# Performance work log

Hardware: AMD Instinct MI355X
Metric: run time of the kernel (lower is better)

The kernel has to match this reference:

```python
import jax, jax.numpy as jnp
import numpy as np

B, N, D_PTS, D_MODEL, K = 2, 8192, 3, 128, 16


def _gather(points, idx):
    # points: (B, N, C), idx: (B, M, K) -> (B, M, K, C)
    return jax.vmap(lambda p, i: p[i])(points, idx)


def setup_inputs() -> dict:
    key = jax.random.key(0)
    ks = jax.random.split(key, 20)

    def w(k, shape, fan_in):
        bound = 1.0 / np.sqrt(fan_in)
        return jax.random.uniform(k, shape, jnp.float32, -bound, bound)

    return {
        "xyz": jax.random.normal(ks[0], (B, D_PTS, N), jnp.float32),
        "features": jax.random.normal(ks[1], (B, D_PTS, N), jnp.float32),
        "fc1_w": w(ks[2], (D_MODEL, D_PTS), D_PTS),
        "fc1_b": w(ks[3], (D_MODEL,), D_PTS),
        "fc2_w": w(ks[4], (D_PTS, D_MODEL), D_MODEL),
        "fc2_b": w(ks[5], (D_PTS,), D_MODEL),
        "d1_w": w(ks[6], (D_MODEL, 3), 3),
        "d1_b": w(ks[7], (D_MODEL,), 3),
        "d2_w": w(ks[8], (D_MODEL, D_MODEL), D_MODEL),
        "d2_b": w(ks[9], (D_MODEL,), D_MODEL),
        "g1_w": w(ks[10], (D_MODEL, D_MODEL), D_MODEL),
        "g1_b": w(ks[11], (D_MODEL,), D_MODEL),
        "g2_w": w(ks[12], (D_MODEL, D_MODEL), D_MODEL),
        "g2_b": w(ks[13], (D_MODEL,), D_MODEL),
        "wq_w": w(ks[14], (D_MODEL, D_MODEL), D_MODEL),
        "wk_w": w(ks[15], (D_MODEL, D_MODEL), D_MODEL),
        "wv_w": w(ks[16], (D_MODEL, D_MODEL), D_MODEL),
    }


def reference(xyz, features, fc1_w, fc1_b, fc2_w, fc2_b,
              d1_w, d1_b, d2_w, d2_b, g1_w, g1_b, g2_w, g2_b,
              wq_w, wk_w, wv_w):
    xyz_p = jnp.swapaxes(xyz, 1, 2)        # (B, N, 3)
    feat = jnp.swapaxes(features, 1, 2)    # (B, N, d_points)

    # square_distance(xyz, xyz): ||a||^2 + ||b||^2 - 2 a.b
    sq = jnp.sum(xyz_p * xyz_p, axis=-1)   # (B, N)
    dists = sq[:, :, None] + sq[:, None, :] - 2.0 * jnp.einsum('bnc,bmc->bnm', xyz_p, xyz_p)
    _, knn_idx = jax.lax.top_k(-dists, K)  # (B, N, K) indices of k smallest dists

    knn_xyz = _gather(xyz_p, knn_idx)      # (B, N, K, 3)
    pre = feat

    x = feat @ fc1_w.T + fc1_b             # (B, N, d_model)
    q = x @ wq_w.T                         # (B, N, d_model)
    kg = _gather(x @ wk_w.T, knn_idx)      # (B, N, K, d_model)
    vg = _gather(x @ wv_w.T, knn_idx)      # (B, N, K, d_model)

    rel = xyz_p[:, :, None] - knn_xyz      # (B, N, K, 3)
    pos = jax.nn.relu(rel @ d1_w.T + d1_b) @ d2_w.T + d2_b          # fc_delta

    h = q[:, :, None] - kg + pos
    attn = jax.nn.relu(h @ g1_w.T + g1_b) @ g2_w.T + g2_b           # fc_gamma
    attn = jax.nn.softmax(attn / np.sqrt(D_MODEL), axis=-2)         # softmax over K

    res = jnp.einsum('bmnf,bmnf->bmf', attn, vg + pos)              # (B, N, d_model)
    res = res @ fc2_w.T + fc2_b + pre                               # (B, N, d_points)
    return jnp.swapaxes(res, 1, 2)                                  # (B, d_points, N)
```

## Files before the change

kernel.cpp:

```cpp
#include <hip/hip_runtime.h>
#include <cfloat>

#define NPTS 8192

typedef __attribute__((ext_vector_type(8))) short short8;
typedef __attribute__((ext_vector_type(4))) short short4v;
typedef __attribute__((ext_vector_type(4))) float f32x4;

__device__ inline unsigned short f2bf(float f) {
    unsigned u = __builtin_bit_cast(unsigned, f);
    u += 0x7fffu + ((u >> 16) & 1u);
    return (unsigned short)(u >> 16);
}
__device__ inline float bf2f(unsigned short h) {
    unsigned u = ((unsigned)h) << 16;
    return __builtin_bit_cast(float, u);
}

__global__ void prep_kernel(const float* __restrict__ d2_w,
                            const float* __restrict__ g1_w,
                            const float* __restrict__ g2_w,
                            unsigned short* __restrict__ wd2,
                            unsigned short* __restrict__ wg1,
                            unsigned short* __restrict__ wg2,
                            const float* __restrict__ xyz,
                            float4* __restrict__ candp,
                            const float* __restrict__ wq_w,
                            const float* __restrict__ wk_w,
                            const float* __restrict__ wv_w,
                            float* __restrict__ wqT,
                            float* __restrict__ wkT,
                            float* __restrict__ wvT)
{
    int i = blockIdx.x * 256 + threadIdx.x;
    if (i < 49152) {
        int sel = i >> 14, off = i & 16383;
        const float* s = (sel == 0) ? d2_w : (sel == 1) ? g1_w : g2_w;
        unsigned short* d = (sel == 0) ? wd2 : (sel == 1) ? wg1 : wg2;
        d[off] = f2bf(s[off]);
    } else if (i < 65536) {
        int j = i - 49152;
        int b = j >> 13, n = j & 8191;
        const float* xg = xyz + (long)b * 3 * NPTS;
        float x = xg[n], y = xg[NPTS + n], z = xg[2*NPTS + n];
        float4 c; c.x = x; c.y = y; c.z = z;
        c.w = fmaf(x, x, fmaf(y, y, z * z));
        candp[j] = c;
    } else if (i < 114688) {
        int idx = i - 65536;
        int sel = idx >> 14, off = idx & 16383;
        int k = off >> 7, c = off & 127;
        const float* s = (sel == 0) ? wq_w : (sel == 1) ? wk_w : wv_w;
        float* d = (sel == 0) ? wqT : (sel == 1) ? wkT : wvT;
        d[off] = s[c * 128 + k];
    }
}

#define KNB 120
#define KBBASE 952
#define KCAP 64

__global__ __launch_bounds__(512, 2)
void knn_proj_kernel(const float4* __restrict__ cand,
                     float* __restrict__ part_d, int* __restrict__ part_i,
                     const float* __restrict__ feat,
                     const float* __restrict__ fc1_w, const float* __restrict__ fc1_b,
                     const float* __restrict__ wqT, const float* __restrict__ wkT,
                     const float* __restrict__ wvT,
                     unsigned short* __restrict__ qb,
                     unsigned short* __restrict__ kbuf,
                     unsigned short* __restrict__ vbuf)
{
    __shared__ union {
        struct {
            unsigned hist[KNB * 64];
            float2   surv[64 * 65];
            unsigned scnt[64];
            int      bthr[64];
        } k;
        struct {
            float fl[32][3];
            float xl[32][128];
        } p;
    } sm;

    const int t = threadIdx.x;

    if (blockIdx.x < 512) {
        unsigned* hist = sm.k.hist;
        float2*   surv = sm.k.surv;
        unsigned* scnt = sm.k.scnt;
        int*      bthr = sm.k.bthr;

        const int ql = t & 63, wv = t >> 6;
        const int wv_u = __builtin_amdgcn_readfirstlane(wv);
        const int qsg = blockIdx.x >> 1;
        const int ck  = blockIdx.x & 1;
        const int b_u = qsg >> 7;
        const int q   = qsg * 64 + ql;
        const int n   = q & 8191;

        const float4* cp = cand + (b_u << 13) + ck * 4096 + wv_u * 512;
        const int ibase = ck * 4096 + wv_u * 512;
        float4 qc = cand[(b_u << 13) + n];
        const float qx2 = -2.f * qc.x, qy2 = -2.f * qc.y, qz2 = -2.f * qc.z;
        const float qw = qc.w;

        for (int i = t; i < KNB * 64; i += 512) hist[i] = 0u;
        if (t < 64) scnt[t] = 0u;
        __syncthreads();

        auto dtil = [&](float4 c) {
            return fmaf(qx2, c.x, fmaf(qy2, c.y, fmaf(qz2, c.z, c.w + qw)));
        };
        auto binOf = [&](float d) {
            float dc = fmaxf(d, 1e-30f);
            int b = (int)(__builtin_bit_cast(unsigned, dc) >> 20) - KBBASE;
            return b < 0 ? 0 : (b > (KNB - 1) ? (KNB - 1) : b);
        };

        {
            unsigned* hq = hist + ql;
            float4 A[8], Bv[8];
            #pragma unroll
            for (int u = 0; u < 8; ++u) A[u] = cp[u];
            for (int m = 0; m < 512; m += 16) {
                #pragma unroll
                for (int u = 0; u < 8; ++u) Bv[u] = cp[m + 8 + u];
                #pragma unroll
                for (int u = 0; u < 8; ++u) {
                    int bb = binOf(dtil(A[u]));
                    atomicAdd(hq + bb * 64, 1u);
                }
                if (m + 16 < 512) {
                    #pragma unroll
                    for (int u = 0; u < 8; ++u) A[u] = cp[m + 16 + u];
                }
                #pragma unroll
                for (int u = 0; u < 8; ++u) {
                    int bb = binOf(dtil(Bv[u]));
                    atomicAdd(hq + bb * 64, 1u);
                }
            }
        }
        __syncthreads();

        if (t < 64) {
            int cum = 0, bs = 0;
            #pragma unroll 8
            for (int b = 0; b < KNB; ++b) {
                cum += (int)hist[b * 64 + t];
                bs += (cum < 16) ? 1 : 0;
            }
            bthr[t] = (bs >= KNB - 1) ? 0x7FFFFFFF : ((bs + KBBASE + 1) << 20);
        }
        __syncthreads();

        {
            const int mythr = bthr[ql];
            float4 A[8], Bv[8];
            #pragma unroll
            for (int u = 0; u < 8; ++u) A[u] = cp[u];
            for (int m = 0; m < 512; m += 16) {
                #pragma unroll
                for (int u = 0; u < 8; ++u) Bv[u] = cp[m + 8 + u];
                #pragma unroll
                for (int u = 0; u < 8; ++u) {
                    float d = dtil(A[u]);
                    if (__builtin_bit_cast(int, d) < mythr) {
                        unsigned s = atomicAdd(&scnt[ql], 1u);
                        if (s < (unsigned)KCAP) {
                            float2 e; e.x = d;
                            e.y = __builtin_bit_cast(float, ibase + m + u);
                            surv[ql * 65 + s] = e;
                        }
                    }
                }
                if (m + 16 < 512) {
                    #pragma unroll
                    for (int u = 0; u < 8; ++u) A[u] = cp[m + 16 + u];
                }
                #pragma unroll
                for (int u = 0; u < 8; ++u) {
                    float d = dtil(Bv[u]);
                    if (__builtin_bit_cast(int, d) < mythr) {
                        unsigned s = atomicAdd(&scnt[ql], 1u);
                        if (s < (unsigned)KCAP) {
                            float2 e; e.x = d;
                            e.y = __builtin_bit_cast(float, ibase + m + 8 + u);
                            surv[ql * 65 + s] = e;
                        }
                    }
                }
            }
        }
        __syncthreads();

        {
            const int q2 = t >> 3;
            const int s0 = t & 7;
            const unsigned cnt = min(scnt[q2], (unsigned)KCAP);
            const float2* sp = surv + q2 * 65;
            const long pb = ((long)(qsg * 64 + q2)) * 32 + ck * 16;
            for (unsigned s = s0; s < cnt; s += 8) {
                float2 e = sp[s];
                float d = e.x;
                int idx = __builtin_bit_cast(int, e.y);
                int rank = 0;
                #pragma unroll 8
                for (unsigned j = 0; j < cnt; ++j) {
                    float2 f = sp[j];
                    float dj = f.x;
                    int ij = __builtin_bit_cast(int, f.y);
                    rank += ((dj < d) || (dj == d && ij < idx)) ? 1 : 0;
                }
                if (rank < 16) {
                    part_d[pb + rank] = d;
                    part_i[pb + rank] = idx;
                }
            }
        }
    } else {
        float (*fl)[3]   = sm.p.fl;
        float (*xl)[128] = sm.p.xl;

        const int tc = t & 127;
        const int pg = t >> 7;
        const long base = (long)(blockIdx.x - 512) * 32 + pg * 8;

        if (tc < 24) {
            int p = tc / 3, d = tc % 3;
            long pt = base + p;
            int b = (int)(pt >> 13), n = (int)(pt & 8191);
            fl[pg*8 + p][d] = feat[((long)b * 3 + d) * NPTS + n];
        }
        __syncthreads();

        float w0 = fc1_w[tc*3+0], w1 = fc1_w[tc*3+1], w2 = fc1_w[tc*3+2];
        float b0 = fc1_b[tc];
        #pragma unroll
        for (int p = 0; p < 8; ++p)
            xl[pg*8 + p][tc] = fmaf(w0, fl[pg*8+p][0],
                               fmaf(w1, fl[pg*8+p][1],
                               fmaf(w2, fl[pg*8+p][2], b0)));
        __syncthreads();

        float aq[8], ak[8], av[8];
        #pragma unroll
        for (int p = 0; p < 8; ++p) { aq[p] = 0.f; ak[p] = 0.f; av[p] = 0.f; }

        for (int i4 = 0; i4 < 32; ++i4) {
            const int k0 = i4 * 4;
            float qa = wqT[(k0+0)*128 + tc], qbw = wqT[(k0+1)*128 + tc];
            float qc2 = wqT[(k0+2)*128 + tc], qd = wqT[(k0+3)*128 + tc];
            float ka = wkT[(k0+0)*128 + tc], kbw = wkT[(k0+1)*128 + tc];
            float kc2 = wkT[(k0+2)*128 + tc], kd = wkT[(k0+3)*128 + tc];
            float va = wvT[(k0+0)*128 + tc], vbw = wvT[(k0+1)*128 + tc];
            float vc2 = wvT[(k0+2)*128 + tc], vd = wvT[(k0+3)*128 + tc];
            #pragma unroll
            for (int p = 0; p < 8; ++p) {
                float4 x = *(const float4*)&xl[pg*8 + p][k0];
                aq[p] = fmaf(qa,x.x, fmaf(qbw,x.y, fmaf(qc2,x.z, fmaf(qd,x.w, aq[p]))));
                ak[p] = fmaf(ka,x.x, fmaf(kbw,x.y, fmaf(kc2,x.z, fmaf(kd,x.w, ak[p]))));
                av[p] = fmaf(va,x.x, fmaf(vbw,x.y, fmaf(vc2,x.z, fmaf(vd,x.w, av[p]))));
            }
        }
        const int perm = (tc & 15) * 8 + (tc >> 4);
        #pragma unroll
        for (int p = 0; p < 8; ++p) {
            long pt = base + p;
            qb[pt*128 + perm]   = f2bf(aq[p]);
            kbuf[pt*128 + perm] = f2bf(ak[p]);
            vbuf[pt*128 + perm] = f2bf(av[p]);
        }
    }
}

__global__ __launch_bounds__(256, 4)
void knn_merge_kernel(const float* __restrict__ part_d,
                      const int* __restrict__ part_i, int* __restrict__ knn)
{
    __shared__ float sd[8][33];
    __shared__ int   si[8][33];
    const int t = threadIdx.x;
    const int qq = t >> 5, e = t & 31;
    const long q = (long)blockIdx.x * 8 + qq;
    float d = part_d[q * 32 + e];
    int idx = part_i[q * 32 + e];
    sd[qq][e] = d; si[qq][e] = idx;
    __syncthreads();
    int rank = 0;
    #pragma unroll
    for (int j = 0; j < 32; ++j) {
        float dj = sd[qq][j];
        rank += ((dj < d) || (dj == d && si[qq][j] < idx)) ? 1 : 0;
    }
    if (rank < 16) knn[q * 16 + rank] = idx;
}

__device__ inline int hswz(int r, int c) {
    return r * 128 + (c ^ ((r & 7) << 4));
}

__global__ __launch_bounds__(64, 2)
void attn_kernel(const float* __restrict__ xyz, const float* __restrict__ feat,
                 const float* __restrict__ d1_w, const float* __restrict__ d1_b,
                 const float* __restrict__ d2_b, const float* __restrict__ g1_b,
                 const float* __restrict__ g2_b,
                 const float* __restrict__ fc2_w, const float* __restrict__ fc2_b,
                 const unsigned short* __restrict__ qb,
                 const unsigned short* __restrict__ kb,
                 const unsigned short* __restrict__ vb,
                 const unsigned short* __restrict__ wd2,
                 const unsigned short* __restrict__ wg1,
                 const unsigned short* __restrict__ wg2,
                 const int* __restrict__ knn, float* __restrict__ out)
{
    __shared__ unsigned short hbuf[32 * 128];

    const int lane = threadIdx.x;
    const int quad = lane >> 4, l15 = lane & 15;
    const long pbase = (long)blockIdx.x * 2;
    const int b = (int)(pbase >> 13);
    const long bofs = (long)b * NPTS;

    int m = 0; float rx = 0.f, ry = 0.f, rz = 0.f;
    if (lane < 32) {
        m = knn[(pbase + (lane >> 4)) * 16 + (lane & 15)];
        int nn = (int)((pbase + (lane >> 4)) & 8191);
        const float* xg = xyz + (long)b * 3 * NPTS;
        rx = xg[nn]        - xg[m];
        ry = xg[NPTS+nn]   - xg[NPTS+m];
        rz = xg[2*NPTS+nn] - xg[2*NPTS+m];
    }

    int koff[8];
    #pragma unroll
    for (int mt = 0; mt < 2; ++mt)
        #pragma unroll
        for (int r = 0; r < 4; ++r) {
            int idxm = __shfl(m, mt*16 + quad*4 + r);
            koff[mt*4 + r] = (int)(bofs + idxm) * 128 + l15*8;
        }

    short8 qvv[2], kgv[2][4], vgv[2][4];
    #pragma unroll
    for (int mt = 0; mt < 2; ++mt) {
        qvv[mt] = *(const short8*)(qb + (size_t)(pbase + mt) * 128 + l15*8);
        #pragma unroll
        for (int r = 0; r < 4; ++r)
            kgv[mt][r] = *(const short8*)(kb + koff[mt*4 + r]);
    }

    {
        float w0[8], w1[8], w2[8], bb[8];
        #pragma unroll
        for (int k = 0; k < 8; ++k) {
            int c = l15*8 + k;
            w0[k] = d1_w[c*3]; w1[k] = d1_w[c*3+1]; w2[k] = d1_w[c*3+2];
            bb[k] = d1_b[c];
        }
        #pragma unroll
        for (int i = 0; i < 8; ++i) {
            int row = quad + 4*i;
            float sx = __shfl(rx, row), sy = __shfl(ry, row), sz = __shfl(rz, row);
            short8 hv;
            #pragma unroll
            for (int k = 0; k < 8; ++k) {
                float v = fmaf(w0[k], sx, fmaf(w1[k], sy, fmaf(w2[k], sz, bb[k])));
                hv[k] = (short)f2bf(fmaxf(v, 0.f));
            }
            *(short8*)&hbuf[hswz(row, l15*8)] = hv;
        }
    }

    short8 A[2][4];
    f32x4 acc[2];

    auto loadA = [&]() {
        #pragma unroll
        for (int mt = 0; mt < 2; ++mt)
            #pragma unroll
            for (int kk = 0; kk < 4; ++kk)
                A[mt][kk] = *(const short8*)&hbuf[hswz(mt*16 + l15, kk*32 + quad*8)];
    };

    unsigned posp[2][8][2];

    loadA();
    #pragma unroll
    for (int n0 = 0; n0 < 8; ++n0) {
        const unsigned short* wp = wd2 + (n0*16 + l15) * 128 + quad*8;
        short8 B0 = *(const short8*)(wp);
        short8 B1 = *(const short8*)(wp + 32);
        short8 B2 = *(const short8*)(wp + 64);
        short8 B3 = *(const short8*)(wp + 96);
        acc[0] = (f32x4){0.f,0.f,0.f,0.f};
        acc[1] = (f32x4){0.f,0.f,0.f,0.f};
        __builtin_amdgcn_s_setprio(1);
        #pragma unroll
        for (int mt = 0; mt < 2; ++mt) {
            acc[mt] = __builtin_amdgcn_mfma_f32_16x16x32_bf16(A[mt][0], B0, acc[mt], 0, 0, 0);
            acc[mt] = __builtin_amdgcn_mfma_f32_16x16x32_bf16(A[mt][1], B1, acc[mt], 0, 0, 0);
            acc[mt] = __builtin_amdgcn_mfma_f32_16x16x32_bf16(A[mt][2], B2, acc[mt], 0, 0, 0);
            acc[mt] = __builtin_amdgcn_mfma_f32_16x16x32_bf16(A[mt][3], B3, acc[mt], 0, 0, 0);
        }
        __builtin_amdgcn_s_setprio(0);
        int c = n0*16 + l15;
        float bb = d2_b[c];
        #pragma unroll
        for (int mt = 0; mt < 2; ++mt) {
            float qv = bf2f((unsigned short)qvv[mt][n0]);
            float p0 = acc[mt][0] + bb, p1 = acc[mt][1] + bb;
            float p2 = acc[mt][2] + bb, p3 = acc[mt][3] + bb;
            posp[mt][n0][0] = (unsigned)f2bf(p0) | ((unsigned)f2bf(p1) << 16);
            posp[mt][n0][1] = (unsigned)f2bf(p2) | ((unsigned)f2bf(p3) << 16);
            int rb = mt*16 + quad*4;
            hbuf[hswz(rb+0, c)] = f2bf(qv - bf2f((unsigned short)kgv[mt][0][n0]) + p0);
            hbuf[hswz(rb+1, c)] = f2bf(qv - bf2f((unsigned short)kgv[mt][1][n0]) + p1);
            hbuf[hswz(rb+2, c)] = f2bf(qv - bf2f((unsigned short)kgv[mt][2][n0]) + p2);
            hbuf[hswz(rb+3, c)] = f2bf(qv - bf2f((unsigned short)kgv[mt][3][n0]) + p3);
        }
    }

    loadA();
    #pragma unroll
    for (int n0 = 0; n0 < 8; ++n0) {
        const unsigned short* wp = wg1 + (n0*16 + l15) * 128 + quad*8;
        short8 B0 = *(const short8*)(wp);
        short8 B1 = *(const short8*)(wp + 32);
        short8 B2 = *(const short8*)(wp + 64);
        short8 B3 = *(const short8*)(wp + 96);
        acc[0] = (f32x4){0.f,0.f,0.f,0.f};
        acc[1] = (f32x4){0.f,0.f,0.f,0.f};
        __builtin_amdgcn_s_setprio(1);
        #pragma unroll
        for (int mt = 0; mt < 2; ++mt) {
            acc[mt] = __builtin_amdgcn_mfma_f32_16x16x32_bf16(A[mt][0], B0, acc[mt], 0, 0, 0);
            acc[mt] = __builtin_amdgcn_mfma_f32_16x16x32_bf16(A[mt][1], B1, acc[mt], 0, 0, 0);
            acc[mt] = __builtin_amdgcn_mfma_f32_16x16x32_bf16(A[mt][2], B2, acc[mt], 0, 0, 0);
            acc[mt] = __builtin_amdgcn_mfma_f32_16x16x32_bf16(A[mt][3], B3, acc[mt], 0, 0, 0);
        }
        __builtin_amdgcn_s_setprio(0);
        int c = n0*16 + l15;
        float bb = g1_b[c];
        #pragma unroll
        for (int mt = 0; mt < 2; ++mt) {
            int rb = mt*16 + quad*4;
            #pragma unroll
            for (int r = 0; r < 4; ++r)
                hbuf[hswz(rb+r, c)] = f2bf(fmaxf(acc[mt][r] + bb, 0.f));
        }
    }

    #pragma unroll
    for (int mt = 0; mt < 2; ++mt)
        #pragma unroll
        for (int r = 0; r < 4; ++r)
            vgv[mt][r] = *(const short8*)(vb + koff[mt*4 + r]);

    loadA();
    const float sc = 0.08838834764831845f;
    float pr[2][3];
    #pragma unroll
    for (int mt = 0; mt < 2; ++mt) { pr[mt][0] = 0.f; pr[mt][1] = 0.f; pr[mt][2] = 0.f; }
    #pragma unroll
    for (int n0 = 0; n0 < 8; ++n0) {
        const unsigned short* wp = wg2 + (n0*16 + l15) * 128 + quad*8;
        short8 B0 = *(const short8*)(wp);
        short8 B1 = *(const short8*)(wp + 32);
        short8 B2 = *(const short8*)(wp + 64);
        short8 B3 = *(const short8*)(wp + 96);
        acc[0] = (f32x4){0.f,0.f,0.f,0.f};
        acc[1] = (f32x4){0.f,0.f,0.f,0.f};
        __builtin_amdgcn_s_setprio(1);
        #pragma unroll
        for (int mt = 0; mt < 2; ++mt) {
            acc[mt] = __builtin_amdgcn_mfma_f32_16x16x32_bf16(A[mt][0], B0, acc[mt], 0, 0, 0);
            acc[mt] = __builtin_amdgcn_mfma_f32_16x16x32_bf16(A[mt][1], B1, acc[mt], 0, 0, 0);
            acc[mt] = __builtin_amdgcn_mfma_f32_16x16x32_bf16(A[mt][2], B2, acc[mt], 0, 0, 0);
            acc[mt] = __builtin_amdgcn_mfma_f32_16x16x32_bf16(A[mt][3], B3, acc[mt], 0, 0, 0);
        }
        __builtin_amdgcn_s_setprio(0);
        int c = n0*16 + l15;
        float bb = g2_b[c];
        float f0 = fc2_w[c];
        float f1 = fc2_w[128 + c];
        float f2 = fc2_w[256 + c];
        #pragma unroll
        for (int mt = 0; mt < 2; ++mt) {
            float e0 = (acc[mt][0] + bb) * sc;
            float e1 = (acc[mt][1] + bb) * sc;
            float e2 = (acc[mt][2] + bb) * sc;
            float e3 = (acc[mt][3] + bb) * sc;
            float mx = fmaxf(fmaxf(e0, e1), fmaxf(e2, e3));
            mx = fmaxf(mx, __shfl_xor(mx, 16));
            mx = fmaxf(mx, __shfl_xor(mx, 32));
            e0 = __expf(e0 - mx); e1 = __expf(e1 - mx);
            e2 = __expf(e2 - mx); e3 = __expf(e3 - mx);
            float ssum = e0 + e1 + e2 + e3;
            ssum += __shfl_xor(ssum, 16);
            ssum += __shfl_xor(ssum, 32);
            float p0 = bf2f((unsigned short)(posp[mt][n0][0] & 0xffff));
            float p1 = bf2f((unsigned short)(posp[mt][n0][0] >> 16));
            float p2 = bf2f((unsigned short)(posp[mt][n0][1] & 0xffff));
            float p3 = bf2f((unsigned short)(posp[mt][n0][1] >> 16));
            float p = e0 * (bf2f((unsigned short)vgv[mt][0][n0]) + p0)
                    + e1 * (bf2f((unsigned short)vgv[mt][1][n0]) + p1)
                    + e2 * (bf2f((unsigned short)vgv[mt][2][n0]) + p2)
                    + e3 * (bf2f((unsigned short)vgv[mt][3][n0]) + p3);
            p += __shfl_xor(p, 16);
            p += __shfl_xor(p, 32);
            float rres = p / ssum;
            pr[mt][0] = fmaf(f0, rres, pr[mt][0]);
            pr[mt][1] = fmaf(f1, rres, pr[mt][1]);
            pr[mt][2] = fmaf(f2, rres, pr[mt][2]);
        }
    }

    #pragma unroll
    for (int mt = 0; mt < 2; ++mt) {
        float pr0 = pr[mt][0], pr1 = pr[mt][1], pr2 = pr[mt][2];
        #pragma unroll
        for (int s2 = 1; s2 <= 8; s2 <<= 1) {
            pr0 += __shfl_xor(pr0, s2);
            pr1 += __shfl_xor(pr1, s2);
            pr2 += __shfl_xor(pr2, s2);
        }
        int nn = (int)((pbase + mt) & 8191);
        if (lane < 3) {
            float pv = (lane == 0) ? pr0 : (lane == 1) ? pr1 : pr2;
            long o = ((long)b*3 + lane) * NPTS + nn;
            out[o] = pv + fc2_b[lane] + feat[o];
        }
    }
}

extern "C" void kernel_launch(void* const* d_in, const int* in_sizes, int n_in,
                              void* d_out, int out_size, void* d_ws, size_t ws_size,
                              hipStream_t stream)
{
    const float* xyz   = (const float*)d_in[0];
    const float* feat  = (const float*)d_in[1];
    const float* fc1_w = (const float*)d_in[2];
    const float* fc1_b = (const float*)d_in[3];
    const float* fc2_w = (const float*)d_in[4];
    const float* fc2_b = (const float*)d_in[5];
    const float* d1_w  = (const float*)d_in[6];
    const float* d1_b  = (const float*)d_in[7];
    const float* d2_w  = (const float*)d_in[8];
    const float* d2_b  = (const float*)d_in[9];
    const float* g1_w  = (const float*)d_in[10];
    const float* g1_b  = (const float*)d_in[11];
    const float* g2_w  = (const float*)d_in[12];
    const float* g2_b  = (const float*)d_in[13];
    const float* wq_w  = (const float*)d_in[14];
    const float* wk_w  = (const float*)d_in[15];
    const float* wv_w  = (const float*)d_in[16];
    float* out = (float*)d_out;

    unsigned short* qb  = (unsigned short*)d_ws;
    unsigned short* kb  = qb + (size_t)16384*128;
    unsigned short* vb  = kb + (size_t)16384*128;
    unsigned short* wd2 = vb + (size_t)16384*128;
    unsigned short* wg1 = wd2 + 16384;
    unsigned short* wg2 = wg1 + 16384;
    int*   knn_ws = (int*)(wg2 + 16384);
    float4* cand  = (float4*)(knn_ws + (size_t)16384*16);
    float* part_d = (float*)(cand + 16384);
    int*   part_i = (int*)(part_d + (size_t)16384*64);
    float* wqT    = part_d + (size_t)16384*32;
    float* wkT    = wqT + 16384;
    float* wvT    = wkT + 16384;

    hipLaunchKernelGGL(prep_kernel, dim3(448), dim3(256), 0, stream,
                       d2_w, g1_w, g2_w, wd2, wg1, wg2, xyz, cand,
                       wq_w, wk_w, wv_w, wqT, wkT, wvT);
    hipLaunchKernelGGL(knn_proj_kernel, dim3(1024), dim3(512), 0, stream,
                       cand, part_d, part_i,
                       feat, fc1_w, fc1_b, wqT, wkT, wvT, qb, kb, vb);
    hipLaunchKernelGGL(knn_merge_kernel, dim3(2048), dim3(256), 0, stream,
                       part_d, part_i, knn_ws);
    hipLaunchKernelGGL(attn_kernel, dim3(8192), dim3(64), 0, stream,
                       xyz, feat, d1_w, d1_b, d2_b, g1_b, g2_b, fc2_w, fc2_b,
                       qb, kb, vb, wd2, wg1, wg2, knn_ws, out);
}
```

Measured before the change: 296.6 us.

## Split KNN partial pass into own kernel and fuse merge with QKV projection

The KNN partial-selection pass moves into its own kernel with launch bounds (512,6) and no shared-memory union with the projection path. The QKV projection blocks, now processing 16 points per 256-thread block, join the KNN merge kernel in a single launch. This lets the KNN kernel run at higher occupancy without carrying the projection's shared-memory footprint. The merge and the projection can overlap in one launch. It trades this against losing the previous overlap of projection with the histogram KNN pass.

```diff
diff --git a/kernel.cpp b/kernel.cpp
--- a/kernel.cpp
+++ b/kernel.cpp
@@ -60,179 +60,188 @@
 #define KBBASE 952
 #define KCAP 64
 
-__global__ __launch_bounds__(512, 2)
-void knn_proj_kernel(const float4* __restrict__ cand,
-                     float* __restrict__ part_d, int* __restrict__ part_i,
-                     const float* __restrict__ feat,
-                     const float* __restrict__ fc1_w, const float* __restrict__ fc1_b,
-                     const float* __restrict__ wqT, const float* __restrict__ wkT,
-                     const float* __restrict__ wvT,
-                     unsigned short* __restrict__ qb,
-                     unsigned short* __restrict__ kbuf,
-                     unsigned short* __restrict__ vbuf)
+__global__ __launch_bounds__(512, 6)
+void knn_part_kernel(const float4* __restrict__ cand,
+                     float* __restrict__ part_d, int* __restrict__ part_i)
+{
+    __shared__ unsigned hist[KNB * 64];
+    __shared__ float2   surv[64 * 65];
+    __shared__ unsigned scnt[64];
+    __shared__ int      bthr[64];
+
+    const int t  = threadIdx.x;
+    const int ql = t & 63, wv = t >> 6;
+    const int wv_u = __builtin_amdgcn_readfirstlane(wv);
+    const int qsg = blockIdx.x >> 1;
+    const int ck  = blockIdx.x & 1;
+    const int b_u = qsg >> 7;
+    const int q   = qsg * 64 + ql;
+    const int n   = q & 8191;
+
+    const float4* cp = cand + (b_u << 13) + ck * 4096 + wv_u * 512;
+    const int ibase = ck * 4096 + wv_u * 512;
+    float4 qc = cand[(b_u << 13) + n];
+    const float qx2 = -2.f * qc.x, qy2 = -2.f * qc.y, qz2 = -2.f * qc.z;
+    const float qw = qc.w;
+
+    for (int i = t; i < KNB * 64; i += 512) hist[i] = 0u;
+    if (t < 64) scnt[t] = 0u;
+    __syncthreads();
+
+    auto dtil = [&](float4 c) {
+        return fmaf(qx2, c.x, fmaf(qy2, c.y, fmaf(qz2, c.z, c.w + qw)));
+    };
+    auto binOf = [&](float d) {
+        float dc = fmaxf(d, 1e-30f);
+        int b = (int)(__builtin_bit_cast(unsigned, dc) >> 20) - KBBASE;
+        return b < 0 ? 0 : (b > (KNB - 1) ? (KNB - 1) : b);
+    };
+
+    {
+        unsigned* hq = hist + ql;
+        float4 A[8], Bv[8];
+        #pragma unroll
+        for (int u = 0; u < 8; ++u) A[u] = cp[u];
+        for (int m = 0; m < 512; m += 16) {
+            #pragma unroll
+            for (int u = 0; u < 8; ++u) Bv[u] = cp[m + 8 + u];
+            #pragma unroll
+            for (int u = 0; u < 8; ++u) {
+                int bb = binOf(dtil(A[u]));
+                atomicAdd(hq + bb * 64, 1u);
+            }
+            if (m + 16 < 512) {
+                #pragma unroll
+                for (int u = 0; u < 8; ++u) A[u] = cp[m + 16 + u];
+            }
+            #pragma unroll
+            for (int u = 0; u < 8; ++u) {
+                int bb = binOf(dtil(Bv[u]));
+                atomicAdd(hq + bb * 64, 1u);
+            }
+        }
+    }
+    __syncthreads();
+
+    if (t < 64) {
+        int cum = 0, bs = 0;
+        #pragma unroll 8
+        for (int b = 0; b < KNB; ++b) {
+            cum += (int)hist[b * 64 + t];
+            bs += (cum < 16) ? 1 : 0;
+        }
+        bthr[t] = (bs >= KNB - 1) ? 0x7FFFFFFF : ((bs + KBBASE + 1) << 20);
+    }
+    __syncthreads();
+
+    {
+        const int mythr = bthr[ql];
+        float4 A[8], Bv[8];
+        #pragma unroll
+        for (int u = 0; u < 8; ++u) A[u] = cp[u];
+        for (int m = 0; m < 512; m += 16) {
+            #pragma unroll
+            for (int u = 0; u < 8; ++u) Bv[u] = cp[m + 8 + u];
+            #pragma unroll
+            for (int u = 0; u < 8; ++u) {
+                float d = dtil(A[u]);
+                if (__builtin_bit_cast(int, d) < mythr) {
+                    unsigned s = atomicAdd(&scnt[ql], 1u);
+                    if (s < (unsigned)KCAP) {
+                        float2 e; e.x = d;
+                        e.y = __builtin_bit_cast(float, ibase + m + u);
+                        surv[ql * 65 + s] = e;
+                    }
+                }
+            }
+            if (m + 16 < 512) {
+                #pragma unroll
+                for (int u = 0; u < 8; ++u) A[u] = cp[m + 16 + u];
+            }
+            #pragma unroll
+            for (int u = 0; u < 8; ++u) {
+                float d = dtil(Bv[u]);
+                if (__builtin_bit_cast(int, d) < mythr) {
+                    unsigned s = atomicAdd(&scnt[ql], 1u);
+                    if (s < (unsigned)KCAP) {
+                        float2 e; e.x = d;
+                        e.y = __builtin_bit_cast(float, ibase + m + 8 + u);
+                        surv[ql * 65 + s] = e;
+                    }
+                }
+            }
+        }
+    }
+    __syncthreads();
+
+    {
+        const int q2 = t >> 3;
+        const int s0 = t & 7;
+        const unsigned cnt = min(scnt[q2], (unsigned)KCAP);
+        const float2* sp = surv + q2 * 65;
+        const long pb = ((long)(qsg * 64 + q2)) * 32 + ck * 16;
+        for (unsigned s = s0; s < cnt; s += 8) {
+            float2 e = sp[s];
+            float d = e.x;
+            int idx = __builtin_bit_cast(int, e.y);
+            int rank = 0;
+            #pragma unroll 8
+            for (unsigned j = 0; j < cnt; ++j) {
+                float2 f = sp[j];
+                float dj = f.x;
+                int ij = __builtin_bit_cast(int, f.y);
+                rank += ((dj < d) || (dj == d && ij < idx)) ? 1 : 0;
+            }
+            if (rank < 16) {
+                part_d[pb + rank] = d;
+                part_i[pb + rank] = idx;
+            }
+        }
+    }
+}
+
+__global__ __launch_bounds__(256, 4)
+void merge_proj_kernel(const float* __restrict__ part_d,
+                       const int* __restrict__ part_i, int* __restrict__ knn,
+                       const float* __restrict__ feat,
+                       const float* __restrict__ fc1_w, const float* __restrict__ fc1_b,
+                       const float* __restrict__ wqT, const float* __restrict__ wkT,
+                       const float* __restrict__ wvT,
+                       unsigned short* __restrict__ qb,
+                       unsigned short* __restrict__ kbuf,
+                       unsigned short* __restrict__ vbuf)
 {
     __shared__ union {
-        struct {
-            unsigned hist[KNB * 64];
-            float2   surv[64 * 65];
-            unsigned scnt[64];
-            int      bthr[64];
-        } k;
-        struct {
-            float fl[32][3];
-            float xl[32][128];
-        } p;
+        struct { float sd[8][33]; int si[8][33]; } m;
+        struct { float fl[16][3]; float xl[16][128]; } p;
     } sm;
 
     const int t = threadIdx.x;
 
-    if (blockIdx.x < 512) {
-        unsigned* hist = sm.k.hist;
-        float2*   surv = sm.k.surv;
-        unsigned* scnt = sm.k.scnt;
-        int*      bthr = sm.k.bthr;
-
-        const int ql = t & 63, wv = t >> 6;
-        const int wv_u = __builtin_amdgcn_readfirstlane(wv);
-        const int qsg = blockIdx.x >> 1;
-        const int ck  = blockIdx.x & 1;
-        const int b_u = qsg >> 7;
-        const int q   = qsg * 64 + ql;
-        const int n   = q & 8191;
-
-        const float4* cp = cand + (b_u << 13) + ck * 4096 + wv_u * 512;
-        const int ibase = ck * 4096 + wv_u * 512;
-        float4 qc = cand[(b_u << 13) + n];
-        const float qx2 = -2.f * qc.x, qy2 = -2.f * qc.y, qz2 = -2.f * qc.z;
-        const float qw = qc.w;
-
-        for (int i = t; i < KNB * 64; i += 512) hist[i] = 0u;
-        if (t < 64) scnt[t] = 0u;
+    if (blockIdx.x < 2048) {
+        const int qq = t >> 5, e = t & 31;
+        const long q = (long)blockIdx.x * 8 + qq;
+        float d = part_d[q * 32 + e];
+        int idx = part_i[q * 32 + e];
+        sm.m.sd[qq][e] = d; sm.m.si[qq][e] = idx;
         __syncthreads();
-
-        auto dtil = [&](float4 c) {
-            return fmaf(qx2, c.x, fmaf(qy2, c.y, fmaf(qz2, c.z, c.w + qw)));
-        };
-        auto binOf = [&](float d) {
-            float dc = fmaxf(d, 1e-30f);
-            int b = (int)(__builtin_bit_cast(unsigned, dc) >> 20) - KBBASE;
-            return b < 0 ? 0 : (b > (KNB - 1) ? (KNB - 1) : b);
-        };
-
-        {
-            unsigned* hq = hist + ql;
-            float4 A[8], Bv[8];
-            #pragma unroll
-            for (int u = 0; u < 8; ++u) A[u] = cp[u];
-            for (int m = 0; m < 512; m += 16) {
-                #pragma unroll
-                for (int u = 0; u < 8; ++u) Bv[u] = cp[m + 8 + u];
-                #pragma unroll
-                for (int u = 0; u < 8; ++u) {
-                    int bb = binOf(dtil(A[u]));
-                    atomicAdd(hq + bb * 64, 1u);
-                }
-                if (m + 16 < 512) {
-                    #pragma unroll
-                    for (int u = 0; u < 8; ++u) A[u] = cp[m + 16 + u];
-                }
-                #pragma unroll
-                for (int u = 0; u < 8; ++u) {
-                    int bb = binOf(dtil(Bv[u]));
-                    atomicAdd(hq + bb * 64, 1u);
-                }
-            }
-        }
-        __syncthreads();
-
-        if (t < 64) {
-            int cum = 0, bs = 0;
-            #pragma unroll 8
-            for (int b = 0; b < KNB; ++b) {
-                cum += (int)hist[b * 64 + t];
-                bs += (cum < 16) ? 1 : 0;
-            }
-            bthr[t] = (bs >= KNB - 1) ? 0x7FFFFFFF : ((bs + KBBASE + 1) << 20);
-        }
-        __syncthreads();
-
-        {
-            const int mythr = bthr[ql];
-            float4 A[8], Bv[8];
-            #pragma unroll
-            for (int u = 0; u < 8; ++u) A[u] = cp[u];
-            for (int m = 0; m < 512; m += 16) {
-                #pragma unroll
-                for (int u = 0; u < 8; ++u) Bv[u] = cp[m + 8 + u];
-                #pragma unroll
-                for (int u = 0; u < 8; ++u) {
-                    float d = dtil(A[u]);
-                    if (__builtin_bit_cast(int, d) < mythr) {
-                        unsigned s = atomicAdd(&scnt[ql], 1u);
-                        if (s < (unsigned)KCAP) {
-                            float2 e; e.x = d;
-                            e.y = __builtin_bit_cast(float, ibase + m + u);
-                            surv[ql * 65 + s] = e;
-                        }
-                    }
-                }
-                if (m + 16 < 512) {
-                    #pragma unroll
-                    for (int u = 0; u < 8; ++u) A[u] = cp[m + 16 + u];
-                }
-                #pragma unroll
-                for (int u = 0; u < 8; ++u) {
-                    float d = dtil(Bv[u]);
-                    if (__builtin_bit_cast(int, d) < mythr) {
-                        unsigned s = atomicAdd(&scnt[ql], 1u);
-                        if (s < (unsigned)KCAP) {
-                            float2 e; e.x = d;
-                            e.y = __builtin_bit_cast(float, ibase + m + 8 + u);
-                            surv[ql * 65 + s] = e;
-                        }
-                    }
-                }
-            }
-        }
-        __syncthreads();
-
-        {
-            const int q2 = t >> 3;
-            const int s0 = t & 7;
-            const unsigned cnt = min(scnt[q2], (unsigned)KCAP);
-            const float2* sp = surv + q2 * 65;
-            const long pb = ((long)(qsg * 64 + q2)) * 32 + ck * 16;
-            for (unsigned s = s0; s < cnt; s += 8) {
-                float2 e = sp[s];
-                float d = e.x;
-                int idx = __builtin_bit_cast(int, e.y);
-                int rank = 0;
-                #pragma unroll 8
-                for (unsigned j = 0; j < cnt; ++j) {
-                    float2 f = sp[j];
-                    float dj = f.x;
-                    int ij = __builtin_bit_cast(int, f.y);
-                    rank += ((dj < d) || (dj == d && ij < idx)) ? 1 : 0;
-                }
-                if (rank < 16) {
-                    part_d[pb + rank] = d;
-                    part_i[pb + rank] = idx;
-                }
-            }
-        }
+        int rank = 0;
+        #pragma unroll
+        for (int j = 0; j < 32; ++j) {
+            float dj = sm.m.sd[qq][j];
+            rank += ((dj < d) || (dj == d && sm.m.si[qq][j] < idx)) ? 1 : 0;
+        }
+        if (rank < 16) knn[q * 16 + rank] = idx;
     } else {
-        float (*fl)[3]   = sm.p.fl;
-        float (*xl)[128] = sm.p.xl;
-
         const int tc = t & 127;
         const int pg = t >> 7;
-        const long base = (long)(blockIdx.x - 512) * 32 + pg * 8;
+        const long base = (long)(blockIdx.x - 2048) * 16 + pg * 8;
 
         if (tc < 24) {
             int p = tc / 3, d = tc % 3;
             long pt = base + p;
             int b = (int)(pt >> 13), n = (int)(pt & 8191);
-            fl[pg*8 + p][d] = feat[((long)b * 3 + d) * NPTS + n];
+            sm.p.fl[pg*8 + p][d] = feat[((long)b * 3 + d) * NPTS + n];
         }
         __syncthreads();
 
@@ -240,9 +249,9 @@
         float b0 = fc1_b[tc];
         #pragma unroll
         for (int p = 0; p < 8; ++p)
-            xl[pg*8 + p][tc] = fmaf(w0, fl[pg*8+p][0],
-                               fmaf(w1, fl[pg*8+p][1],
-                               fmaf(w2, fl[pg*8+p][2], b0)));
+            sm.p.xl[pg*8 + p][tc] = fmaf(w0, sm.p.fl[pg*8+p][0],
+                                    fmaf(w1, sm.p.fl[pg*8+p][1],
+                                    fmaf(w2, sm.p.fl[pg*8+p][2], b0)));
         __syncthreads();
 
         float aq[8], ak[8], av[8];
@@ -259,7 +268,7 @@
             float vc2 = wvT[(k0+2)*128 + tc], vd = wvT[(k0+3)*128 + tc];
             #pragma unroll
             for (int p = 0; p < 8; ++p) {
-                float4 x = *(const float4*)&xl[pg*8 + p][k0];
+                float4 x = *(const float4*)&sm.p.xl[pg*8 + p][k0];
                 aq[p] = fmaf(qa,x.x, fmaf(qbw,x.y, fmaf(qc2,x.z, fmaf(qd,x.w, aq[p]))));
                 ak[p] = fmaf(ka,x.x, fmaf(kbw,x.y, fmaf(kc2,x.z, fmaf(kd,x.w, ak[p]))));
                 av[p] = fmaf(va,x.x, fmaf(vbw,x.y, fmaf(vc2,x.z, fmaf(vd,x.w, av[p]))));
@@ -274,28 +283,6 @@
             vbuf[pt*128 + perm] = f2bf(av[p]);
         }
     }
-}
-
-__global__ __launch_bounds__(256, 4)
-void knn_merge_kernel(const float* __restrict__ part_d,
-                      const int* __restrict__ part_i, int* __restrict__ knn)
-{
-    __shared__ float sd[8][33];
-    __shared__ int   si[8][33];
-    const int t = threadIdx.x;
-    const int qq = t >> 5, e = t & 31;
-    const long q = (long)blockIdx.x * 8 + qq;
-    float d = part_d[q * 32 + e];
-    int idx = part_i[q * 32 + e];
-    sd[qq][e] = d; si[qq][e] = idx;
-    __syncthreads();
-    int rank = 0;
-    #pragma unroll
-    for (int j = 0; j < 32; ++j) {
-        float dj = sd[qq][j];
-        rank += ((dj < d) || (dj == d && si[qq][j] < idx)) ? 1 : 0;
-    }
-    if (rank < 16) knn[q * 16 + rank] = idx;
 }
 
 __device__ inline int hswz(int r, int c) {
@@ -576,11 +563,11 @@
     hipLaunchKernelGGL(prep_kernel, dim3(448), dim3(256), 0, stream,
                        d2_w, g1_w, g2_w, wd2, wg1, wg2, xyz, cand,
                        wq_w, wk_w, wv_w, wqT, wkT, wvT);
-    hipLaunchKernelGGL(knn_proj_kernel, dim3(1024), dim3(512), 0, stream,
-                       cand, part_d, part_i,
+    hipLaunchKernelGGL(knn_part_kernel, dim3(512), dim3(512), 0, stream,
+                       cand, part_d, part_i);
+    hipLaunchKernelGGL(merge_proj_kernel, dim3(3072), dim3(256), 0, stream,
+                       part_d, part_i, knn_ws,
                        feat, fc1_w, fc1_b, wqT, wkT, wvT, qb, kb, vb);
-    hipLaunchKernelGGL(knn_merge_kernel, dim3(2048), dim3(256), 0, stream,
-                       part_d, part_i, knn_ws);
     hipLaunchKernelGGL(attn_kernel, dim3(8192), dim3(64), 0, stream,
                        xyz, feat, d1_w, d1_b, d2_b, g1_b, g2_b, fc2_w, fc2_b,
                        qb, kb, vb, wd2, wg1, wg2, knn_ws, out);
```

Result: slower. 320.6 us (+8.1%).
